# Kernel optimization log

Measured on AMD Instinct MI355X. Metric: run time of the kernel, lower is better.

## Reference

```python
import jax, jax.numpy as jnp
from jax import lax
import numpy as np

K = 3        # adaptive kernel size
STRIDE = 1
PAD = (K - 1) // 2


def setup_inputs() -> dict:
    key = jax.random.key(0)
    ks = jax.random.split(key, 10)
    N, C, H, W = 32, 512, 56, 56
    Cm, P = 128, 512  # Cm = inplanes // m, P = planes

    def rn(k, shape, scale=0.05):
        return jax.random.normal(k, shape, dtype=jnp.float32) * scale

    return dict(
        x=jax.random.normal(ks[0], (N, C, H, W), dtype=jnp.float32),
        conv_w=rn(ks[1], (Cm, C)),      # self.conv 1x1 weight (squeezed)
        conv_b=rn(ks[2], (Cm,)),        # self.conv bias
        ck_w=rn(ks[3], (K * K,)),       # self.conv_kernel 1x1 weight (1 in-ch)
        ck_b=rn(ks[4], (K * K,)),       # self.conv_kernel bias
        ckk_w=rn(ks[5], (Cm,)),         # self.conv_k 1x1 weight (1 in-ch)
        ckk_b=rn(ks[6], (Cm,)),         # self.conv_k bias
        adap_b=rn(ks[7], (Cm,)),        # self.conv_adap_kernel bias (weight is generated)
        fuse_w=rn(ks[8], (P, Cm)),      # self.fuse 1x1 weight (squeezed)
        fuse_b=rn(ks[9], (P,)),         # self.fuse bias
    )


def _forward(x, conv_w, conv_b, ck_w, ck_b, ckk_w, ckk_b, adap_b, fuse_w, fuse_b):
    N, C, H, W = x.shape
    Cm = conv_w.shape[0]

    # f = relu(conv(x)) : [N, Cm, H, W]
    f = jax.nn.relu(jnp.einsum('nchw,oc->nohw', x, conv_w) + conv_b[None, :, None, None])

    # g = relu(conv(avg_pool(x))) : [N, Cm]  (spatial dims are 1x1, squeezed)
    pooled = jnp.mean(x, axis=(2, 3))                       # [N, C]
    g = jax.nn.relu(pooled @ conv_w.T + conv_b)             # [N, Cm]

    # conv_kernel (1x1, 1->k*k channels) applied on permuted g:
    # ker[n, ic, kk] = ck_w[kk] * g[n, ic] + ck_b[kk]
    ker = g[:, :, None] * ck_w[None, None, :] + ck_b[None, None, :]   # [N, Cm, k*k]

    # conv_k (1x1, 1->Cm channels) generates per-sample dynamic conv weights:
    # Wk[n, oc, ic, kk] = relu(ckk_w[oc] * ker[n, ic, kk] + ckk_b[oc])
    Wk = jax.nn.relu(ckk_w[None, :, None, None] * ker[:, None, :, :]
                     + ckk_b[None, :, None, None])          # [N, Cm, Cm, k*k]
    Wk = Wk.reshape(N, Cm, Cm, K, K)                        # per-sample OIHW weights

    # Per-sample dynamic conv, batched with vmap (replaces the python loop + weight swap)
    def dyn_conv(f_n, w_n):  # f_n: [Cm,H,W], w_n: [Cm,Cm,K,K]
        return lax.conv_general_dilated(
            f_n[None], w_n, (STRIDE, STRIDE), [(PAD, PAD), (PAD, PAD)],
            dimension_numbers=('NCHW', 'OIHW', 'NCHW'))[0]

    y = jax.vmap(dyn_conv)(f, Wk) + adap_b[None, :, None, None]  # [N, Cm, H, W]

    # fuse 1x1 conv: Cm -> planes
    out = jnp.einsum('nchw,pc->nphw', y, fuse_w) + fuse_b[None, :, None, None]
    return out


def reference(x, conv_w, conv_b, ck_w, ck_b, ckk_w, ckk_b, adap_b, fuse_w, fuse_b):
    return _forward(x, conv_w, conv_b, ck_w, ck_b, ckk_w, ckk_b, adap_b, fuse_w, fuse_b)
```

## Files before the change

kernel.cpp:

```cpp
#include <hip/hip_runtime.h>

#define N_   32
#define C_   512
#define HW_  3136
#define W_   56
#define H_   56
#define CM_  128
#define P_   512

typedef __attribute__((ext_vector_type(8))) short bf16x8;
typedef __attribute__((ext_vector_type(4))) float f32x4;

__device__ inline ushort f2bf(float x) {
    unsigned u = __float_as_uint(x);
    u += 0x7fff + ((u >> 16) & 1);
    return (ushort)(u >> 16);
}

__global__ __launch_bounds__(256) void prep_w(const float* __restrict__ conv_w,
                                              const float* __restrict__ fuse_w,
                                              ushort* __restrict__ Acv,
                                              ushort* __restrict__ Afu) {
    int idx = blockIdx.x * 256 + threadIdx.x;
    if (idx < 65536) {
        int ci = idx & 7, cm = (idx >> 3) & 127, cb = idx >> 10;
        Acv[idx] = f2bf(conv_w[cm * C_ + cb * 8 + ci]);
    } else {
        int j = idx - 65536;
        int ci = j & 7, p = (j >> 3) & 511, kb = j >> 12;
        Afu[j] = f2bf(fuse_w[p * CM_ + kb * 8 + ci]);
    }
}

__global__ __launch_bounds__(256) void transpose_cast(const float* __restrict__ x,
                                                      ushort* __restrict__ x_t,
                                                      float* __restrict__ pooled) {
    int pixbase = blockIdx.x * 64, c0 = blockIdx.y * 64, n = blockIdx.z;
    __shared__ float tile[64 * 65];
    int t = threadIdx.x;
    const float inv = 1.0f / (float)HW_;
    #pragma unroll
    for (int it = 0; it < 4; it++) {
        int c = it * 16 + (t >> 4), p4 = (t & 15) * 4;
        float4 v = *(const float4*)&x[((size_t)(n * C_ + c0 + c)) * HW_ + pixbase + p4];
        tile[c * 65 + p4]     = v.x;
        tile[c * 65 + p4 + 1] = v.y;
        tile[c * 65 + p4 + 2] = v.z;
        tile[c * 65 + p4 + 3] = v.w;
        float s = v.x + v.y + v.z + v.w;
        s += __shfl_down(s, 8, 16);
        s += __shfl_down(s, 4, 16);
        s += __shfl_down(s, 2, 16);
        s += __shfl_down(s, 1, 16);
        if ((t & 15) == 0) atomicAdd(&pooled[n * C_ + c0 + c], s * inv);
    }
    __syncthreads();
    int pix = t >> 2, part = t & 3;
    unsigned pk[8];
    #pragma unroll
    for (int i = 0; i < 16; i += 2) {
        ushort lo = f2bf(tile[(part * 16 + i) * 65 + pix]);
        ushort hi = f2bf(tile[(part * 16 + i + 1) * 65 + pix]);
        pk[i >> 1] = (unsigned)lo | ((unsigned)hi << 16);
    }
    ushort* dst = &x_t[((size_t)(n * HW_ + pixbase + pix)) * C_ + c0 + part * 16];
    *(uint4*)dst       = make_uint4(pk[0], pk[1], pk[2], pk[3]);
    *(uint4*)(dst + 8) = make_uint4(pk[4], pk[5], pk[6], pk[7]);
}

__global__ __launch_bounds__(128) void g_kernel(const float* __restrict__ pooled,
                                                const float* __restrict__ conv_w,
                                                const float* __restrict__ conv_b,
                                                float* __restrict__ g) {
    int n = blockIdx.x, o = threadIdx.x;
    __shared__ float ps[C_];
    for (int c = threadIdx.x; c < C_; c += 128) ps[c] = pooled[n * C_ + c];
    __syncthreads();
    float acc = conv_b[o];
    for (int c = 0; c < C_; c++) acc += ps[c] * conv_w[o * C_ + c];
    g[n * CM_ + o] = fmaxf(acc, 0.f);
}

__global__ __launch_bounds__(256) void wk_frag(const float* __restrict__ g,
                                               const float* __restrict__ ck_w,
                                               const float* __restrict__ ck_b,
                                               const float* __restrict__ ckk_w,
                                               const float* __restrict__ ckk_b,
                                               ushort* __restrict__ Wkf) {
    int idx = blockIdx.x * 256 + threadIdx.x;
    int ci = idx & 7, oc = (idx >> 3) & 127, icb = (idx >> 10) & 15, rest = idx >> 14;
    int kk = rest % 9, n = rest / 9;
    int ic = icb * 8 + ci;
    float ker = ck_w[kk] * g[n * CM_ + ic] + ck_b[kk];
    Wkf[idx] = f2bf(fmaxf(ckk_w[oc] * ker + ckk_b[oc], 0.f));
}

__global__ __launch_bounds__(256) void gemm_f(const ushort* __restrict__ x_t,
                                              const ushort* __restrict__ Acv,
                                              const float* __restrict__ conv_b,
                                              ushort* __restrict__ f_t) {
    int pixbase = blockIdx.x * 64, n = blockIdx.z;
    int t = threadIdx.x, wv = t >> 6, lane = t & 63, col = lane & 15, quad = lane >> 4;
    __shared__ ushort bsh[64 * 40];
    f32x4 z = {0.f, 0.f, 0.f, 0.f};
    f32x4 acc[2][4];
    #pragma unroll
    for (int mt = 0; mt < 2; mt++)
        #pragma unroll
        for (int ns = 0; ns < 4; ns++) acc[mt][ns] = z;
    int spix = t >> 2, sch = t & 3;
    const ushort* srcbase = &x_t[((size_t)(n * HW_ + pixbase + spix)) * C_ + sch * 8];
    for (int cb0 = 0; cb0 < 16; cb0++) {
        *(uint4*)&bsh[spix * 40 + sch * 8] = *(const uint4*)(srcbase + cb0 * 32);
        __syncthreads();
        bf16x8 a[2], b[4];
        #pragma unroll
        for (int mt = 0; mt < 2; mt++)
            a[mt] = *(const bf16x8*)&Acv[(((cb0 * 4 + quad) * CM_) + wv * 32 + mt * 16 + col) * 8];
        #pragma unroll
        for (int ns = 0; ns < 4; ns++)
            b[ns] = *(const bf16x8*)&bsh[(ns * 16 + col) * 40 + quad * 8];
        #pragma unroll
        for (int mt = 0; mt < 2; mt++)
            #pragma unroll
            for (int ns = 0; ns < 4; ns++)
                acc[mt][ns] = __builtin_amdgcn_mfma_f32_16x16x32_bf16(a[mt], b[ns], acc[mt][ns], 0, 0, 0);
        __syncthreads();
    }
    #pragma unroll
    for (int mt = 0; mt < 2; mt++) {
        int ocr = wv * 32 + mt * 16 + quad * 4;
        float b0 = conv_b[ocr], b1 = conv_b[ocr + 1], b2 = conv_b[ocr + 2], b3 = conv_b[ocr + 3];
        #pragma unroll
        for (int ns = 0; ns < 4; ns++) {
            int pix = pixbase + ns * 16 + col;
            ushort4 o;
            o.x = f2bf(fmaxf(acc[mt][ns][0] + b0, 0.f));
            o.y = f2bf(fmaxf(acc[mt][ns][1] + b1, 0.f));
            o.z = f2bf(fmaxf(acc[mt][ns][2] + b2, 0.f));
            o.w = f2bf(fmaxf(acc[mt][ns][3] + b3, 0.f));
            *(ushort4*)&f_t[((size_t)(n * HW_ + pix)) * CM_ + ocr] = o;
        }
    }
}

__global__ __launch_bounds__(256) void gemm_dyn(const ushort* __restrict__ f_t,
                                                const ushort* __restrict__ Wkf,
                                                const float* __restrict__ adap_b,
                                                ushort* __restrict__ y_t) {
    int pixbase = blockIdx.x * 64, n = blockIdx.z;
    int t = threadIdx.x, wv = t >> 6, lane = t & 63, col = lane & 15, quad = lane >> 4;
    int h_lo = pixbase / W_;
    __shared__ ushort fsh[232 * 40];
    int ldspix[4];
    #pragma unroll
    for (int ns = 0; ns < 4; ns++) {
        int pix = pixbase + ns * 16 + col;
        int h = pix / W_, w = pix - h * W_;
        ldspix[ns] = (h - h_lo) * 58 + w;
    }
    f32x4 acc[2][4];
    #pragma unroll
    for (int mt = 0; mt < 2; mt++) {
        int ocr = wv * 32 + mt * 16 + quad * 4;
        f32x4 ab = {adap_b[ocr], adap_b[ocr + 1], adap_b[ocr + 2], adap_b[ocr + 3]};
        #pragma unroll
        for (int ns = 0; ns < 4; ns++) acc[mt][ns] = ab;
    }
    for (int ic0 = 0; ic0 < CM_; ic0 += 32) {
        #pragma unroll
        for (int it = 0; it < 4; it++) {
            int idx = it * 256 + t;
            if (idx < 928) {
                int lp = idx >> 2, ch = idx & 3;
                int r = lp / 58, cw = lp - r * 58;
                int hp = h_lo + r;
                uint4 v = {0u, 0u, 0u, 0u};
                if (hp >= 1 && hp <= H_ && cw >= 1 && cw <= W_)
                    v = *(const uint4*)&f_t[((size_t)(n * HW_ + (hp - 1) * W_ + cw - 1)) * CM_ + ic0 + ch * 8];
                *(uint4*)&fsh[lp * 40 + ch * 8] = v;
            }
        }
        __syncthreads();
        #pragma unroll
        for (int dh = 0; dh < 3; dh++) {
            #pragma unroll
            for (int dw = 0; dw < 3; dw++) {
                int kk = dh * 3 + dw;
                bf16x8 a[2], b[4];
                #pragma unroll
                for (int mt = 0; mt < 2; mt++)
                    a[mt] = *(const bf16x8*)&Wkf[((((size_t)(n * 9 + kk) * 16) + (ic0 >> 3) + quad) * CM_ + wv * 32 + mt * 16 + col) * 8];
                #pragma unroll
                for (int ns = 0; ns < 4; ns++)
                    b[ns] = *(const bf16x8*)&fsh[(ldspix[ns] + dh * 58 + dw) * 40 + quad * 8];
                #pragma unroll
                for (int mt = 0; mt < 2; mt++)
                    #pragma unroll
                    for (int ns = 0; ns < 4; ns++)
                        acc[mt][ns] = __builtin_amdgcn_mfma_f32_16x16x32_bf16(a[mt], b[ns], acc[mt][ns], 0, 0, 0);
            }
        }
        __syncthreads();
    }
    #pragma unroll
    for (int mt = 0; mt < 2; mt++) {
        int ocr = wv * 32 + mt * 16 + quad * 4;
        #pragma unroll
        for (int ns = 0; ns < 4; ns++) {
            int pix = pixbase + ns * 16 + col;
            ushort4 o;
            o.x = f2bf(acc[mt][ns][0]);
            o.y = f2bf(acc[mt][ns][1]);
            o.z = f2bf(acc[mt][ns][2]);
            o.w = f2bf(acc[mt][ns][3]);
            *(ushort4*)&y_t[((size_t)(n * HW_ + pix)) * CM_ + ocr] = o;
        }
    }
}

__global__ __launch_bounds__(256) void gemm_fuse(const ushort* __restrict__ y_t,
                                                 const ushort* __restrict__ Afu,
                                                 const float* __restrict__ fuse_b,
                                                 float* __restrict__ out) {
    int pixbase = blockIdx.x * 64, pbase = blockIdx.y * 128, n = blockIdx.z;
    int t = threadIdx.x, wv = t >> 6, lane = t & 63, col = lane & 15, quad = lane >> 4;
    __shared__ ushort bsh[64 * 40];
    f32x4 z = {0.f, 0.f, 0.f, 0.f};
    f32x4 acc[2][4];
    #pragma unroll
    for (int mt = 0; mt < 2; mt++)
        #pragma unroll
        for (int ns = 0; ns < 4; ns++) acc[mt][ns] = z;
    int spix = t >> 2, sch = t & 3;
    const ushort* srcbase = &y_t[((size_t)(n * HW_ + pixbase + spix)) * CM_ + sch * 8];
    for (int cb0 = 0; cb0 < 4; cb0++) {
        *(uint4*)&bsh[spix * 40 + sch * 8] = *(const uint4*)(srcbase + cb0 * 32);
        __syncthreads();
        bf16x8 a[2], b[4];
        #pragma unroll
        for (int mt = 0; mt < 2; mt++)
            a[mt] = *(const bf16x8*)&Afu[(((cb0 * 4 + quad) * P_) + pbase + wv * 32 + mt * 16 + col) * 8];
        #pragma unroll
        for (int ns = 0; ns < 4; ns++)
            b[ns] = *(const bf16x8*)&bsh[(ns * 16 + col) * 40 + quad * 8];
        #pragma unroll
        for (int mt = 0; mt < 2; mt++)
            #pragma unroll
            for (int ns = 0; ns < 4; ns++)
                acc[mt][ns] = __builtin_amdgcn_mfma_f32_16x16x32_bf16(a[mt], b[ns], acc[mt][ns], 0, 0, 0);
        __syncthreads();
    }
    #pragma unroll
    for (int mt = 0; mt < 2; mt++) {
        int pr = pbase + wv * 32 + mt * 16 + quad * 4;
        #pragma unroll
        for (int ns = 0; ns < 4; ns++) {
            int pix = pixbase + ns * 16 + col;
            #pragma unroll
            for (int r = 0; r < 4; r++)
                out[((size_t)(n * P_ + pr + r)) * HW_ + pix] = acc[mt][ns][r] + fuse_b[pr + r];
        }
    }
}

extern "C" void kernel_launch(void* const* d_in, const int* in_sizes, int n_in,
                              void* d_out, int out_size, void* d_ws, size_t ws_size,
                              hipStream_t stream) {
    const float* x      = (const float*)d_in[0];
    const float* conv_w = (const float*)d_in[1];
    const float* conv_b = (const float*)d_in[2];
    const float* ck_w   = (const float*)d_in[3];
    const float* ck_b   = (const float*)d_in[4];
    const float* ckk_w  = (const float*)d_in[5];
    const float* ckk_b  = (const float*)d_in[6];
    const float* adap_b = (const float*)d_in[7];
    const float* fuse_w = (const float*)d_in[8];
    const float* fuse_b = (const float*)d_in[9];
    float* out = (float*)d_out;

    ushort* x_t = (ushort*)d_ws;
    ushort* y_t = x_t;
    ushort* f_t = x_t + (size_t)51380224;
    ushort* Wkf = f_t + (size_t)12845056;
    ushort* Acv = Wkf + (size_t)4718592;
    ushort* Afu = Acv + (size_t)65536;
    float* pooled = (float*)(Afu + (size_t)65536);
    float* g      = pooled + 16384;

    hipMemsetAsync(pooled, 0, 16384 * sizeof(float), stream);
    prep_w<<<512, 256, 0, stream>>>(conv_w, fuse_w, Acv, Afu);
    transpose_cast<<<dim3(49, 8, N_), 256, 0, stream>>>(x, x_t, pooled);
    g_kernel<<<N_, 128, 0, stream>>>(pooled, conv_w, conv_b, g);
    wk_frag<<<18432, 256, 0, stream>>>(g, ck_w, ck_b, ckk_w, ckk_b, Wkf);
    gemm_f<<<dim3(49, 1, N_), 256, 0, stream>>>(x_t, Acv, conv_b, f_t);
    gemm_dyn<<<dim3(49, 1, N_), 256, 0, stream>>>(f_t, Wkf, adap_b, y_t);
    gemm_fuse<<<dim3(49, 4, N_), 256, 0, stream>>>(y_t, Afu, fuse_b, out);
}
```

Measured before the change: 516.1 us.

## Fuse transpose-cast into conv GEMM and derive pooled g from GEMM sums

The conv 1x1 GEMM now reads fp32 NCHW input directly, converting to bf16 in registers and staging into a double-buffered LDS tile. This removes the separate transpose_cast pass and the bf16 x_t round trip through memory. The pooled branch uses linearity, conv(mean(x)) = mean(conv(x)): per-channel sums of the pre-bias GEMM accumulators are atomically added, and wk_frag applies the scale, bias and relu, which drops g_kernel. The tradeoff is that the pooled value now comes from bf16-rounded products, and the per-thread global loads are strided by channel across HW. Each load is still coalesced across pixels.

```diff
diff --git a/kernel.cpp b/kernel.cpp
--- a/kernel.cpp
+++ b/kernel.cpp
@@ -32,56 +32,108 @@
     }
 }
 
-__global__ __launch_bounds__(256) void transpose_cast(const float* __restrict__ x,
-                                                      ushort* __restrict__ x_t,
-                                                      float* __restrict__ pooled) {
-    int pixbase = blockIdx.x * 64, c0 = blockIdx.y * 64, n = blockIdx.z;
-    __shared__ float tile[64 * 65];
-    int t = threadIdx.x;
-    const float inv = 1.0f / (float)HW_;
-    #pragma unroll
-    for (int it = 0; it < 4; it++) {
-        int c = it * 16 + (t >> 4), p4 = (t & 15) * 4;
-        float4 v = *(const float4*)&x[((size_t)(n * C_ + c0 + c)) * HW_ + pixbase + p4];
-        tile[c * 65 + p4]     = v.x;
-        tile[c * 65 + p4 + 1] = v.y;
-        tile[c * 65 + p4 + 2] = v.z;
-        tile[c * 65 + p4 + 3] = v.w;
-        float s = v.x + v.y + v.z + v.w;
-        s += __shfl_down(s, 8, 16);
-        s += __shfl_down(s, 4, 16);
-        s += __shfl_down(s, 2, 16);
-        s += __shfl_down(s, 1, 16);
-        if ((t & 15) == 0) atomicAdd(&pooled[n * C_ + c0 + c], s * inv);
-    }
+__global__ __launch_bounds__(256) void gemm_f(const float* __restrict__ x,
+                                              const ushort* __restrict__ Acv,
+                                              const float* __restrict__ conv_b,
+                                              ushort* __restrict__ f_t,
+                                              float* __restrict__ gacc) {
+    int pixbase = blockIdx.x * 64, n = blockIdx.z;
+    int t = threadIdx.x, wv = t >> 6, lane = t & 63, col = lane & 15, quad = lane >> 4;
+    __shared__ ushort bsh[2][64 * 40];
+    f32x4 z = {0.f, 0.f, 0.f, 0.f};
+    f32x4 acc[2][4];
+    #pragma unroll
+    for (int mt = 0; mt < 2; mt++)
+        #pragma unroll
+        for (int ns = 0; ns < 4; ns++) acc[mt][ns] = z;
+
+    int spix = t >> 2, chq = (t & 3) * 8;
+    const float* xb = &x[(size_t)n * C_ * HW_ + pixbase + spix];
+
+    float v[8];
+#define LOADV(c0)                                                              \
+    {                                                                          \
+        const float* xs = xb + (size_t)(c0) * HW_;                             \
+        _Pragma("unroll")                                                      \
+        for (int i = 0; i < 8; i++) v[i] = xs[(size_t)(chq + i) * HW_];        \
+    }
+#define PACKW(buf)                                                             \
+    {                                                                          \
+        unsigned p0 = (unsigned)f2bf(v[0]) | ((unsigned)f2bf(v[1]) << 16);     \
+        unsigned p1 = (unsigned)f2bf(v[2]) | ((unsigned)f2bf(v[3]) << 16);     \
+        unsigned p2 = (unsigned)f2bf(v[4]) | ((unsigned)f2bf(v[5]) << 16);     \
+        unsigned p3 = (unsigned)f2bf(v[6]) | ((unsigned)f2bf(v[7]) << 16);     \
+        *(uint4*)&bsh[buf][spix * 40 + chq] = make_uint4(p0, p1, p2, p3);      \
+    }
+
+    LOADV(0);
+    PACKW(0);
     __syncthreads();
-    int pix = t >> 2, part = t & 3;
-    unsigned pk[8];
-    #pragma unroll
-    for (int i = 0; i < 16; i += 2) {
-        ushort lo = f2bf(tile[(part * 16 + i) * 65 + pix]);
-        ushort hi = f2bf(tile[(part * 16 + i + 1) * 65 + pix]);
-        pk[i >> 1] = (unsigned)lo | ((unsigned)hi << 16);
-    }
-    ushort* dst = &x_t[((size_t)(n * HW_ + pixbase + pix)) * C_ + c0 + part * 16];
-    *(uint4*)dst       = make_uint4(pk[0], pk[1], pk[2], pk[3]);
-    *(uint4*)(dst + 8) = make_uint4(pk[4], pk[5], pk[6], pk[7]);
-}
-
-__global__ __launch_bounds__(128) void g_kernel(const float* __restrict__ pooled,
-                                                const float* __restrict__ conv_w,
-                                                const float* __restrict__ conv_b,
-                                                float* __restrict__ g) {
-    int n = blockIdx.x, o = threadIdx.x;
-    __shared__ float ps[C_];
-    for (int c = threadIdx.x; c < C_; c += 128) ps[c] = pooled[n * C_ + c];
-    __syncthreads();
-    float acc = conv_b[o];
-    for (int c = 0; c < C_; c++) acc += ps[c] * conv_w[o * C_ + c];
-    g[n * CM_ + o] = fmaxf(acc, 0.f);
-}
-
-__global__ __launch_bounds__(256) void wk_frag(const float* __restrict__ g,
+    int cur = 0;
+    for (int cb0 = 0; cb0 < 16; cb0++) {
+        if (cb0 < 15) {
+            LOADV((cb0 + 1) * 32);
+            PACKW(cur ^ 1);
+        }
+        bf16x8 a[2], b[4];
+        #pragma unroll
+        for (int mt = 0; mt < 2; mt++)
+            a[mt] = *(const bf16x8*)&Acv[(((cb0 * 4 + quad) * CM_) + wv * 32 + mt * 16 + col) * 8];
+        #pragma unroll
+        for (int ns = 0; ns < 4; ns++)
+            b[ns] = *(const bf16x8*)&bsh[cur][(ns * 16 + col) * 40 + quad * 8];
+        #pragma unroll
+        for (int mt = 0; mt < 2; mt++)
+            #pragma unroll
+            for (int ns = 0; ns < 4; ns++)
+                acc[mt][ns] = __builtin_amdgcn_mfma_f32_16x16x32_bf16(a[mt], b[ns], acc[mt][ns], 0, 0, 0);
+        __syncthreads();
+        cur ^= 1;
+    }
+#undef LOADV
+#undef PACKW
+
+    #pragma unroll
+    for (int mt = 0; mt < 2; mt++) {
+        float ps0 = acc[mt][0][0] + acc[mt][1][0] + acc[mt][2][0] + acc[mt][3][0];
+        float ps1 = acc[mt][0][1] + acc[mt][1][1] + acc[mt][2][1] + acc[mt][3][1];
+        float ps2 = acc[mt][0][2] + acc[mt][1][2] + acc[mt][2][2] + acc[mt][3][2];
+        float ps3 = acc[mt][0][3] + acc[mt][1][3] + acc[mt][2][3] + acc[mt][3][3];
+        #pragma unroll
+        for (int off = 1; off < 16; off <<= 1) {
+            ps0 += __shfl_xor(ps0, off);
+            ps1 += __shfl_xor(ps1, off);
+            ps2 += __shfl_xor(ps2, off);
+            ps3 += __shfl_xor(ps3, off);
+        }
+        if (col == 0) {
+            int ocr = wv * 32 + mt * 16 + quad * 4;
+            atomicAdd(&gacc[n * CM_ + ocr],     ps0);
+            atomicAdd(&gacc[n * CM_ + ocr + 1], ps1);
+            atomicAdd(&gacc[n * CM_ + ocr + 2], ps2);
+            atomicAdd(&gacc[n * CM_ + ocr + 3], ps3);
+        }
+    }
+
+    #pragma unroll
+    for (int mt = 0; mt < 2; mt++) {
+        int ocr = wv * 32 + mt * 16 + quad * 4;
+        float b0 = conv_b[ocr], b1 = conv_b[ocr + 1], b2 = conv_b[ocr + 2], b3 = conv_b[ocr + 3];
+        #pragma unroll
+        for (int ns = 0; ns < 4; ns++) {
+            int pix = pixbase + ns * 16 + col;
+            ushort4 o;
+            o.x = f2bf(fmaxf(acc[mt][ns][0] + b0, 0.f));
+            o.y = f2bf(fmaxf(acc[mt][ns][1] + b1, 0.f));
+            o.z = f2bf(fmaxf(acc[mt][ns][2] + b2, 0.f));
+            o.w = f2bf(fmaxf(acc[mt][ns][3] + b3, 0.f));
+            *(ushort4*)&f_t[((size_t)(n * HW_ + pix)) * CM_ + ocr] = o;
+        }
+    }
+}
+
+__global__ __launch_bounds__(256) void wk_frag(const float* __restrict__ gacc,
+                                               const float* __restrict__ conv_b,
                                                const float* __restrict__ ck_w,
                                                const float* __restrict__ ck_b,
                                                const float* __restrict__ ckk_w,
@@ -91,57 +143,9 @@
     int ci = idx & 7, oc = (idx >> 3) & 127, icb = (idx >> 10) & 15, rest = idx >> 14;
     int kk = rest % 9, n = rest / 9;
     int ic = icb * 8 + ci;
-    float ker = ck_w[kk] * g[n * CM_ + ic] + ck_b[kk];
+    float gv = fmaxf(gacc[n * CM_ + ic] * (1.0f / (float)HW_) + conv_b[ic], 0.f);
+    float ker = ck_w[kk] * gv + ck_b[kk];
     Wkf[idx] = f2bf(fmaxf(ckk_w[oc] * ker + ckk_b[oc], 0.f));
-}
-
-__global__ __launch_bounds__(256) void gemm_f(const ushort* __restrict__ x_t,
-                                              const ushort* __restrict__ Acv,
-                                              const float* __restrict__ conv_b,
-                                              ushort* __restrict__ f_t) {
-    int pixbase = blockIdx.x * 64, n = blockIdx.z;
-    int t = threadIdx.x, wv = t >> 6, lane = t & 63, col = lane & 15, quad = lane >> 4;
-    __shared__ ushort bsh[64 * 40];
-    f32x4 z = {0.f, 0.f, 0.f, 0.f};
-    f32x4 acc[2][4];
-    #pragma unroll
-    for (int mt = 0; mt < 2; mt++)
-        #pragma unroll
-        for (int ns = 0; ns < 4; ns++) acc[mt][ns] = z;
-    int spix = t >> 2, sch = t & 3;
-    const ushort* srcbase = &x_t[((size_t)(n * HW_ + pixbase + spix)) * C_ + sch * 8];
-    for (int cb0 = 0; cb0 < 16; cb0++) {
-        *(uint4*)&bsh[spix * 40 + sch * 8] = *(const uint4*)(srcbase + cb0 * 32);
-        __syncthreads();
-        bf16x8 a[2], b[4];
-        #pragma unroll
-        for (int mt = 0; mt < 2; mt++)
-            a[mt] = *(const bf16x8*)&Acv[(((cb0 * 4 + quad) * CM_) + wv * 32 + mt * 16 + col) * 8];
-        #pragma unroll
-        for (int ns = 0; ns < 4; ns++)
-            b[ns] = *(const bf16x8*)&bsh[(ns * 16 + col) * 40 + quad * 8];
-        #pragma unroll
-        for (int mt = 0; mt < 2; mt++)
-            #pragma unroll
-            for (int ns = 0; ns < 4; ns++)
-                acc[mt][ns] = __builtin_amdgcn_mfma_f32_16x16x32_bf16(a[mt], b[ns], acc[mt][ns], 0, 0, 0);
-        __syncthreads();
-    }
-    #pragma unroll
-    for (int mt = 0; mt < 2; mt++) {
-        int ocr = wv * 32 + mt * 16 + quad * 4;
-        float b0 = conv_b[ocr], b1 = conv_b[ocr + 1], b2 = conv_b[ocr + 2], b3 = conv_b[ocr + 3];
-        #pragma unroll
-        for (int ns = 0; ns < 4; ns++) {
-            int pix = pixbase + ns * 16 + col;
-            ushort4 o;
-            o.x = f2bf(fmaxf(acc[mt][ns][0] + b0, 0.f));
-            o.y = f2bf(fmaxf(acc[mt][ns][1] + b1, 0.f));
-            o.z = f2bf(fmaxf(acc[mt][ns][2] + b2, 0.f));
-            o.w = f2bf(fmaxf(acc[mt][ns][3] + b3, 0.f));
-            *(ushort4*)&f_t[((size_t)(n * HW_ + pix)) * CM_ + ocr] = o;
-        }
-    }
 }
 
 __global__ __launch_bounds__(256) void gemm_dyn(const ushort* __restrict__ f_t,
@@ -279,21 +283,17 @@
     const float* fuse_b = (const float*)d_in[9];
     float* out = (float*)d_out;
 
-    ushort* x_t = (ushort*)d_ws;
-    ushort* y_t = x_t;
-    ushort* f_t = x_t + (size_t)51380224;
+    ushort* y_t = (ushort*)d_ws;
+    ushort* f_t = y_t + (size_t)12845056;
     ushort* Wkf = f_t + (size_t)12845056;
     ushort* Acv = Wkf + (size_t)4718592;
     ushort* Afu = Acv + (size_t)65536;
-    float* pooled = (float*)(Afu + (size_t)65536);
-    float* g      = pooled + 16384;
-
-    hipMemsetAsync(pooled, 0, 16384 * sizeof(float), stream);
+    float* gacc = (float*)(Afu + (size_t)65536);
+
+    hipMemsetAsync(gacc, 0, 4096 * sizeof(float), stream);
     prep_w<<<512, 256, 0, stream>>>(conv_w, fuse_w, Acv, Afu);
-    transpose_cast<<<dim3(49, 8, N_), 256, 0, stream>>>(x, x_t, pooled);
-    g_kernel<<<N_, 128, 0, stream>>>(pooled, conv_w, conv_b, g);
-    wk_frag<<<18432, 256, 0, stream>>>(g, ck_w, ck_b, ckk_w, ckk_b, Wkf);
-    gemm_f<<<dim3(49, 1, N_), 256, 0, stream>>>(x_t, Acv, conv_b, f_t);
+    gemm_f<<<dim3(49, 1, N_), 256, 0, stream>>>(x, Acv, conv_b, f_t, gacc);
+    wk_frag<<<18432, 256, 0, stream>>>(gacc, conv_b, ck_w, ck_b, ckk_w, ckk_b, Wkf);
     gemm_dyn<<<dim3(49, 1, N_), 256, 0, stream>>>(f_t, Wkf, adap_b, y_t);
     gemm_fuse<<<dim3(49, 4, N_), 256, 0, stream>>>(y_t, Afu, fuse_b, out);
 }
```

After: 463.8 us. -10.1%, faster.
